# Performance work log

Measured on AMD Instinct MI355X. Metric: run time of the kernel, lower is better.

The kernel has to match this reference:

```python
import jax, jax.numpy as jnp
import numpy as np

TEMP = 0.07
MAX_SAMPLES = 2048
RADIUS = 10
HARD_FRAC = 0.75
FG_LABEL = 1
B, C, H, W = 8, 64, 256, 256
BLOCK = 32

MAX_FG = MAX_SAMPLES // 2                      # 1024
NEG_BUDGET = MAX_SAMPLES - MAX_FG              # 1024
HARD_BUDGET = int(round(HARD_FRAC * NEG_BUDGET))  # 768
RAND_BUDGET = NEG_BUDGET - HARD_BUDGET         # 256


def setup_inputs() -> dict:
    key = jax.random.key(0)
    feats = jax.random.normal(key, (B, C, H, W), dtype=jnp.float32)
    # 32x32-block checkerboard labels: guarantees abundant fg / ring / interior-bg pools
    ii, jj = jnp.meshgrid(jnp.arange(H), jnp.arange(W), indexing='ij')
    lbl = (((ii // BLOCK) + (jj // BLOCK)) % 2).astype(jnp.int32)
    labels = jnp.broadcast_to(lbl, (B, H, W))
    return {"feats": feats, "labels": labels}


def _forward(feats, labels):
    Bn, Cn, Hn, Wn = feats.shape
    n_pix = Hn * Wn
    f_flat = feats.reshape(Bn, Cn, n_pix).transpose(0, 2, 1)  # [B, P, C]
    l_flat = labels.reshape(Bn, n_pix)

    fg = labels == FG_LABEL                                   # [B, H, W]
    k = 2 * RADIUS + 1
    # max-pool dilation of fg mask (kernel k, stride 1, pad RADIUS == SAME)
    dil = jax.lax.reduce_window(fg.astype(jnp.float32), -jnp.inf, jax.lax.max,
                                (1, k, k), (1, 1, 1), 'SAME') > 0.0
    fg_flat = fg.reshape(Bn, n_pix)
    bg_flat = ~fg_flat                                        # all pixels valid (no ignore)
    ring_flat = dil.reshape(Bn, n_pix) & ~fg_flat & bg_flat
    bgonly_flat = bg_flat & ~ring_flat

    def per_image(f, y, fgm, ringm, bgm, key):
        k1, k2, k3 = jax.random.split(key, 3)
        def pick(mask, kk, n):
            # random subset of n true positions (== randperm[:n] in distribution)
            s = jnp.where(mask, jax.random.uniform(kk, mask.shape), -1.0)
            return jax.lax.top_k(s, n)[1]
        idx = jnp.concatenate([pick(fgm, k1, MAX_FG),
                               pick(ringm, k2, HARD_BUDGET),
                               pick(bgm, k3, RAND_BUDGET)])    # [K]
        fs = f[idx]                                            # [K, C]
        ys = y[idx]
        fs = fs / jnp.maximum(jnp.linalg.norm(fs, axis=1, keepdims=True), 1e-12)
        logits = fs @ fs.T / TEMP                              # [K, K]
        logits = logits - jax.lax.stop_gradient(logits.max(axis=1, keepdims=True))
        eye = jnp.eye(MAX_SAMPLES, dtype=bool)
        pos = (ys[:, None] == ys[None, :]) & ~eye
        exp_l = jnp.exp(logits) * (~eye)
        denom = jnp.maximum(exp_l.sum(axis=1), 1e-8)
        pos_sum = jnp.maximum(jnp.where(pos, exp_l, 0.0).sum(axis=1), 1e-8)
        valid = pos.any(axis=1) & (ys == FG_LABEL)
        loss_terms = -jnp.log(pos_sum / denom)
        n_valid = jnp.maximum(valid.sum(), 1)
        return jnp.where(valid, loss_terms, 0.0).sum() / n_valid

    keys = jax.random.split(jax.random.key(1), Bn)
    losses = jax.vmap(per_image)(f_flat, l_flat, fg_flat, ring_flat, bgonly_flat, keys)
    return losses.mean()


def reference(feats, labels):
    return _forward(feats, labels)
```

## Files before the change

### kernel.cpp

```cpp
#include <hip/hip_runtime.h>
#include <stdint.h>

#define NPIX   65536
#define NIMG   8
#define NCH    64
#define KSEL   2048
#define NFG    1024
#define NRING  768
#define NBG    256
#define INV_TEMP 14.285714285714286f

typedef __attribute__((ext_vector_type(8))) short bf16x8;
typedef __attribute__((ext_vector_type(4))) float f32x4;

__device__ __forceinline__ void tf2x32(uint32_t k0, uint32_t k1,
                                       uint32_t& x0, uint32_t& x1) {
  const uint32_t ks2 = k0 ^ k1 ^ 0x1BD11BDAu;
  x0 += k0; x1 += k1;
#define TF_RND(r) { x0 += x1; x1 = (x1 << (r)) | (x1 >> (32 - (r))); x1 ^= x0; }
  TF_RND(13) TF_RND(15) TF_RND(26) TF_RND(6)
  x0 += k1;  x1 += ks2 + 1u;
  TF_RND(17) TF_RND(29) TF_RND(16) TF_RND(24)
  x0 += ks2; x1 += k0 + 2u;
  TF_RND(13) TF_RND(15) TF_RND(26) TF_RND(6)
  x0 += k0;  x1 += k1 + 3u;
  TF_RND(17) TF_RND(29) TF_RND(16) TF_RND(24)
  x0 += k1;  x1 += ks2 + 4u;
  TF_RND(13) TF_RND(15) TF_RND(26) TF_RND(6)
  x0 += ks2; x1 += k0 + 5u;
#undef TF_RND
}

__device__ __forceinline__ ushort f2bf(float f) {
  uint32_t u = __float_as_uint(f);
  return (ushort)((u + 0x7FFFu + ((u >> 16) & 1u)) >> 16);
}

#define ZERO_F4 1552
__global__ __launch_bounds__(1024) void dilate_pack(const int* __restrict__ labels,
                                                    uint64_t* __restrict__ fgw,
                                                    uint64_t* __restrict__ dilw,
                                                    float4* __restrict__ zregion,
                                                    uint32_t* __restrict__ keys,
                                                    float* __restrict__ out) {
  __shared__ uint64_t fgs[336], hds[336];
  const int tid = threadIdx.x;
  const int img = blockIdx.x >> 2;
  const int r0 = (blockIdx.x & 3) * 64;

  if (blockIdx.x == 0) {
    for (int t = tid; t < ZERO_F4; t += 1024)
      zregion[t] = make_float4(0.f, 0.f, 0.f, 0.f);
  } else if (blockIdx.x == 1 && tid == 0) {
    out[0] = 0.0f;
    for (int b = 0; b < NIMG; ++b) {
      uint32_t kb0 = 0u, kb1 = (uint32_t)b;
      tf2x32(0u, 1u, kb0, kb1);
      for (int g = 0; g < 3; ++g) {
        uint32_t x0 = 0u, x1 = (uint32_t)g;
        tf2x32(kb0, kb1, x0, x1);
        keys[(b * 3 + g) * 2 + 0] = x0;
        keys[(b * 3 + g) * 2 + 1] = x1;
      }
    }
  }

  #pragma unroll
  for (int it = 0; it < 21; ++it) {
    int li = it * 1024 + tid;
    int hr = r0 - 10 + (li >> 8);
    int col = li & 255;
    bool bit = false;
    if (hr >= 0 && hr < 256) bit = (labels[(img << 16) + (hr << 8) + col] == 1);
    uint64_t m = __ballot(bit);
    if ((tid & 63) == 0) fgs[li >> 6] = m;
  }
  __syncthreads();

  for (int w = tid; w < 336; w += 1024) {
    int wc = w & 3;
    uint64_t x = fgs[w];
    uint64_t L = wc > 0 ? fgs[w - 1] : 0ull;
    uint64_t R = wc < 3 ? fgs[w + 1] : 0ull;
    uint64_t acc = x;
    #pragma unroll
    for (int s = 1; s <= 10; ++s) {
      acc |= (x << s) | (L >> (64 - s));
      acc |= (x >> s) | (R << (64 - s));
    }
    hds[w] = acc;
  }
  __syncthreads();

  for (int w = tid; w < 256; w += 1024) {
    int r = w >> 2, wc = w & 3;
    int gr = r0 + r;
    uint64_t acc = 0ull;
    #pragma unroll
    for (int dr = 0; dr <= 20; ++dr) acc |= hds[(r + dr) * 4 + wc];
    fgw[img * 1024 + gr * 4 + wc]  = fgs[(r + 10) * 4 + wc];
    dilw[img * 1024 + gr * 4 + wc] = acc;
  }
}

__global__ __launch_bounds__(256) void hash_hist(const uint64_t* __restrict__ fgw,
                                                 const uint64_t* __restrict__ dilw,
                                                 const uint32_t* __restrict__ keys,
                                                 uint32_t* __restrict__ mgrp,
                                                 uint32_t* __restrict__ hist) {
  __shared__ uint32_t lh[768];
  __shared__ uint64_t fgl[32], dll[32];
  const int tid = threadIdx.x;
  for (int t = tid; t < 768; t += 256) lh[t] = 0;
  const int b = blockIdx.x >> 5;
  const int base = blockIdx.x * 2048;
  const int w0 = (blockIdx.x & 31) * 32;
  if (tid < 32) fgl[tid] = fgw[b * 1024 + w0 + tid];
  else if (tid < 64) dll[tid - 32] = dilw[b * 1024 + w0 + tid - 32];
  const uint32_t K00 = keys[b * 6 + 0], K01 = keys[b * 6 + 1];
  const uint32_t K10 = keys[b * 6 + 2], K11 = keys[b * 6 + 3];
  const uint32_t K20 = keys[b * 6 + 4], K21 = keys[b * 6 + 5];
  __syncthreads();

  #pragma unroll
  for (int k = 0; k < 8; ++k) {
    int off = k * 256 + tid;
    int pix = (base + off) & 65535;
    int lw = off >> 6, bp = off & 63;
    uint32_t fgbit = (uint32_t)((fgl[lw] >> bp) & 1ull);
    uint32_t dilbit = (uint32_t)((dll[lw] >> bp) & 1ull);
    uint32_t grp = fgbit ? 0u : (dilbit ? 1u : 2u);
    uint32_t k0 = grp == 0 ? K00 : grp == 1 ? K10 : K20;
    uint32_t k1 = grp == 0 ? K01 : grp == 1 ? K11 : K21;
    uint32_t x0 = 0u, x1 = (uint32_t)pix;
    tf2x32(k0, k1, x0, x1);
    uint32_t m = (x0 ^ x1) >> 9;
    mgrp[base + off] = (m << 2) | grp;
    atomicAdd(&lh[grp * 256 + (m >> 15)], 1u);
  }
  __syncthreads();
  for (int t = tid; t < 768; t += 256)
    if (lh[t]) atomicAdd(&hist[b * 768 + t], lh[t]);
}

__global__ __launch_bounds__(256) void topk_emit(const uint32_t* __restrict__ mgrp,
                                                 const uint32_t* __restrict__ hist,
                                                 uint32_t* __restrict__ TG,
                                                 uint32_t* __restrict__ cnt,
                                                 uint32_t* __restrict__ candcnt,
                                                 unsigned long long* __restrict__ cand,
                                                 int* __restrict__ idx_out) {
  __shared__ uint32_t hh[768];
  __shared__ uint32_t sT[3], loc[3], lbd[3], basA[3], basB[3];
  const int tid = threadIdx.x;
  const int b = blockIdx.x >> 5;
  const int base = blockIdx.x * 2048;
  for (int t = tid; t < 768; t += 256) hh[t] = hist[b * 768 + t];
  if (tid < 3) { loc[tid] = 0; lbd[tid] = 0; }
  __syncthreads();

  if (tid < 3) {
    uint32_t nsel = tid == 0 ? NFG : tid == 1 ? NRING : NBG;
    const uint32_t* h = hh + tid * 256;
    uint32_t cum = 0; int T = 255;
    for (; T > 0; --T) {
      uint32_t c = h[T];
      if (cum + c >= nsel) break;
      cum += c;
    }
    sT[tid] = (uint32_t)T;
    if ((blockIdx.x & 31) == 0) {
      TG[(b * 3 + tid) * 2] = (uint32_t)T;
      TG[(b * 3 + tid) * 2 + 1] = cum;
    }
  }
  __syncthreads();
  const uint32_t T0 = sT[0], T1 = sT[1], T2 = sT[2];

  #pragma unroll
  for (int k = 0; k < 8; ++k) {
    uint32_t v = mgrp[base + k * 256 + tid];
    uint32_t g = v & 3u, bin = v >> 17;
    uint32_t T = g == 0 ? T0 : g == 1 ? T1 : T2;
    if (bin > T) atomicAdd(&loc[g], 1u);
    else if (bin == T) atomicAdd(&lbd[g], 1u);
  }
  __syncthreads();
  if (tid < 3) {
    basA[tid] = atomicAdd(&cnt[b * 3 + tid], loc[tid]);
    basB[tid] = atomicAdd(&candcnt[b * 3 + tid], lbd[tid]);
    loc[tid] = 0; lbd[tid] = 0;
  }
  __syncthreads();

  #pragma unroll
  for (int k = 0; k < 8; ++k) {
    int p = base + k * 256 + tid;
    uint32_t v = mgrp[p];
    uint32_t g = v & 3u, bin = v >> 17;
    uint32_t T = g == 0 ? T0 : g == 1 ? T1 : T2;
    int pix = p & 65535;
    if (bin > T) {
      uint32_t o = atomicAdd(&loc[g], 1u);
      int seg = g == 0 ? 0 : g == 1 ? NFG : (NFG + NRING);
      idx_out[b * KSEL + seg + (int)(basA[g] + o)] = pix;
    } else if (bin == T) {
      uint32_t o = atomicAdd(&lbd[g], 1u);
      uint32_t c = basB[g] + o;
      uint32_t m = v >> 2;
      if (c < 1024u)
        cand[(b * 3 + g) * 1024 + c] = ((unsigned long long)m << 16) | (uint32_t)pix;
    }
  }
}

#define GA 16
__global__ __launch_bounds__(256) void gather_rank_t(
    const float* __restrict__ feats, const int* __restrict__ idx,
    const uint32_t* __restrict__ TG, const uint32_t* __restrict__ candcnt,
    const unsigned long long* __restrict__ cand, ushort* __restrict__ fs) {
  __shared__ float tile[GA * 65];
  __shared__ float ssb[16 * GA];
  __shared__ float sscale[GA];
  __shared__ int lidx[GA];
  __shared__ unsigned long long cb[1024];
  const int tid = threadIdx.x;
  const int img = blockIdx.x >> 7;
  const int win = (blockIdx.x & 127) * GA;
  int seg, segoff, nsel;
  if (win < NFG)               { seg = 0; segoff = 0;            nsel = NFG; }
  else if (win < NFG + NRING)  { seg = 1; segoff = NFG;          nsel = NRING; }
  else                         { seg = 2; segoff = NFG + NRING;  nsel = NBG; }
  const int task = img * 3 + seg;
  const uint32_t G = TG[task * 2 + 1];
  const int poslo = win - segoff;

  if (tid < GA) {
    if ((uint32_t)(poslo + tid) < G)
      lidx[tid] = idx[img * KSEL + win + tid];
  }
  const bool needRank = (uint32_t)(poslo + GA) > G;
  if (needRank) {
    const int c = (int)(candcnt[task] < 1024u ? candcnt[task] : 1024u);
    const int r = nsel - (int)G;
    for (int i = tid; i < c; i += 256) cb[i] = cand[task * 1024 + i];
    __syncthreads();
    for (int i = tid; i < c; i += 256) {
      unsigned long long me = cb[i];
      uint32_t mm = (uint32_t)(me >> 16), pi = (uint32_t)(me & 0xFFFFu);
      int rank = 0;
      for (int j = 0; j < c; ++j) {
        unsigned long long o = cb[j];
        uint32_t om = (uint32_t)(o >> 16), op = (uint32_t)(o & 0xFFFFu);
        if (om > mm || (om == mm && op < pi)) ++rank;
      }
      if (rank < r) {
        int slot = (int)G + rank - poslo;
        if (slot >= 0 && slot < GA) lidx[slot] = (int)pi;
      }
    }
  }
  __syncthreads();

  const int a = tid & 15, q = tid >> 4;
  const int pix = lidx[a];
  const float* fb = feats + ((size_t)img * NCH + q * 4) * NPIX + pix;
  float ss = 0.f;
  #pragma unroll
  for (int k = 0; k < 4; ++k) {
    float v = fb[(size_t)k * NPIX];
    tile[a * 65 + q * 4 + k] = v;
    ss += v * v;
  }
  ssb[q * GA + a] = ss;
  __syncthreads();
  if (q == 0) {
    float tot = 0.f;
    #pragma unroll
    for (int q2 = 0; q2 < 16; ++q2) tot += ssb[q2 * GA + a];
    sscale[a] = 1.0f / fmaxf(sqrtf(tot), 1e-12f);
  }
  __syncthreads();

  const int row = tid >> 4, c4 = tid & 15;
  const float sc = sscale[row];
  ushort4 v4;
  v4.x = f2bf(tile[row * 65 + c4 * 4 + 0] * sc);
  v4.y = f2bf(tile[row * 65 + c4 * 4 + 1] * sc);
  v4.z = f2bf(tile[row * 65 + c4 * 4 + 2] * sc);
  v4.w = f2bf(tile[row * 65 + c4 * 4 + 3] * sc);
  ((ushort4*)(fs + ((size_t)img * KSEL + win + row) * NCH))[c4] = v4;
}

__global__ __launch_bounds__(256) void loss_mfma(const ushort* __restrict__ fs,
                                                 float* __restrict__ out) {
  const int img = blockIdx.x & 7;
  const int a0 = (blockIdx.x >> 3) * 32;
  const ushort* X = fs + (size_t)img * KSEL * NCH;
  const int tid = threadIdx.x;
  const int lane = tid & 63, wave = tid >> 6;
  const int quad = lane >> 4, col = lane & 15;
  const int rt = wave >> 1, colh = wave & 1;

  __shared__ float redD[2][2][16];
  __shared__ float redP[2][16];

  const int arow = a0 + rt * 16 + col;
  const bf16x8* Ap = (const bf16x8*)(X + (size_t)arow * NCH + quad * 8);
  const bf16x8 a_lo = Ap[0];
  const bf16x8 a_hi = Ap[4];

  float pD[4] = {0.f, 0.f, 0.f, 0.f};
  float pP[4] = {0.f, 0.f, 0.f, 0.f};
  const int ct0 = colh * 64;
  const int mbase = a0 + rt * 16 + quad * 4;

  for (int ct = ct0; ct < ct0 + 64; ++ct) {
    const int j = ct * 16 + col;
    const bf16x8* Bp = (const bf16x8*)(X + (size_t)j * NCH + quad * 8);
    bf16x8 b_lo = Bp[0];
    bf16x8 b_hi = Bp[4];
    f32x4 d = {0.f, 0.f, 0.f, 0.f};
    d = __builtin_amdgcn_mfma_f32_16x16x32_bf16(a_lo, b_lo, d, 0, 0, 0);
    d = __builtin_amdgcn_mfma_f32_16x16x32_bf16(a_hi, b_hi, d, 0, 0, 0);
    #pragma unroll
    for (int r = 0; r < 4; ++r) {
      float e = __expf(d[r] * INV_TEMP);
      if (j == mbase + r) e = 0.f;
      pD[r] += e;
      if (colh == 0) pP[r] += e;
    }
  }

  #pragma unroll
  for (int o = 1; o < 16; o <<= 1) {
    #pragma unroll
    for (int r = 0; r < 4; ++r) {
      pD[r] += __shfl_xor(pD[r], o);
      pP[r] += __shfl_xor(pP[r], o);
    }
  }
  if (col == 0) {
    #pragma unroll
    for (int r = 0; r < 4; ++r) {
      redD[rt][colh][quad * 4 + r] = pD[r];
      if (colh == 0) redP[rt][quad * 4 + r] = pP[r];
    }
  }
  __syncthreads();

  float term = 0.f;
  if (tid < 32) {
    int lrt = tid >> 4, lr = tid & 15;
    float dsum = fmaxf(redD[lrt][0][lr] + redD[lrt][1][lr], 1e-8f);
    float psum = fmaxf(redP[lrt][lr], 1e-8f);
    term = __logf(dsum) - __logf(psum);
  }
  if (tid < 64) {
    #pragma unroll
    for (int o = 32; o > 0; o >>= 1) term += __shfl_xor(term, o);
    if (tid == 0) atomicAdd(out, term * (1.0f / (NFG * NIMG)));
  }
}

extern "C" void kernel_launch(void* const* d_in, const int* in_sizes, int n_in,
                              void* d_out, int out_size, void* d_ws, size_t ws_size,
                              hipStream_t stream) {
  const float* feats = (const float*)d_in[0];
  const int* labels  = (const int*)d_in[1];
  float* out = (float*)d_out;

  char* ws = (char*)d_ws;
  uint64_t* fgw     = (uint64_t*)(ws);
  uint64_t* dilw    = (uint64_t*)(ws + 65536);
  uint32_t* keys    = (uint32_t*)(ws + 131072);
  uint32_t* TG      = (uint32_t*)(ws + 131328);
  uint32_t* hist    = (uint32_t*)(ws + 131584);
  uint32_t* cnt     = (uint32_t*)(ws + 156160);
  uint32_t* candcnt = (uint32_t*)(ws + 156288);
  unsigned long long* cand = (unsigned long long*)(ws + 156416);
  int*      idx     = (int*)(ws + 353024);
  uint32_t* mgrp    = (uint32_t*)(ws + 524288);
  ushort*   fs      = (ushort*)(ws + 2621440);

  hipLaunchKernelGGL(dilate_pack, dim3(32), dim3(1024), 0, stream,
                     labels, fgw, dilw, (float4*)hist, keys, out);
  hipLaunchKernelGGL(hash_hist, dim3(NIMG * 32), dim3(256), 0, stream,
                     fgw, dilw, keys, mgrp, hist);
  hipLaunchKernelGGL(topk_emit, dim3(NIMG * 32), dim3(256), 0, stream,
                     mgrp, hist, TG, cnt, candcnt, cand, idx);
  hipLaunchKernelGGL(gather_rank_t, dim3((NIMG * KSEL) / GA), dim3(256), 0, stream,
                     feats, idx, TG, candcnt, cand, fs);
  hipLaunchKernelGGL(loss_mfma, dim3(NIMG * (NFG / 32)), dim3(256), 0, stream,
                     fs, out);
}
```

Before: 243.0 us.

## Fuse dilation into hashing and replace random gather with streaming compaction

Merges the dilation and hash/histogram kernels into one per-band kernel with per-block histograms in place of global atomics. Instead of scattered per-pixel feature gathers, topk now writes a pixel-to-slot map. A new kernel streams every feature plane coalesced and scatters the selected values into a compact buffer, and a normalise kernel reads that buffer and writes bf16 rows. This trades random 4-byte reads across 64 strided channels for reading the whole 134MB feature tensor sequentially, plus a larger zeroing pass for the map.

```diff
diff --git a/kernel.cpp b/kernel.cpp
--- a/kernel.cpp
+++ b/kernel.cpp
@@ -9,6 +9,10 @@
 #define NRING  768
 #define NBG    256
 #define INV_TEMP 14.285714285714286f
+
+#define FTC    5120
+#define ZERO_F4 65552
+#define ZERO_PER_BLK 257
 
 typedef __attribute__((ext_vector_type(8))) short bf16x8;
 typedef __attribute__((ext_vector_type(4))) float f32x4;
@@ -36,48 +40,47 @@
   return (ushort)((u + 0x7FFFu + ((u >> 16) & 1u)) >> 16);
 }
 
-#define ZERO_F4 1552
-__global__ __launch_bounds__(1024) void dilate_pack(const int* __restrict__ labels,
-                                                    uint64_t* __restrict__ fgw,
-                                                    uint64_t* __restrict__ dilw,
-                                                    float4* __restrict__ zregion,
-                                                    uint32_t* __restrict__ keys,
-                                                    float* __restrict__ out) {
-  __shared__ uint64_t fgs[336], hds[336];
+__global__ __launch_bounds__(256) void prep_hash(const int* __restrict__ labels,
+                                                 float4* __restrict__ zreg,
+                                                 uint32_t* __restrict__ mgrp,
+                                                 uint32_t* __restrict__ hist32,
+                                                 float* __restrict__ out) {
+  __shared__ uint64_t fgs[112], hds[112], fgb[32], dlb[32];
+  __shared__ uint32_t lh[768];
+  __shared__ uint32_t skeys[6];
   const int tid = threadIdx.x;
-  const int img = blockIdx.x >> 2;
-  const int r0 = (blockIdx.x & 3) * 64;
-
-  if (blockIdx.x == 0) {
-    for (int t = tid; t < ZERO_F4; t += 1024)
-      zregion[t] = make_float4(0.f, 0.f, 0.f, 0.f);
-  } else if (blockIdx.x == 1 && tid == 0) {
-    out[0] = 0.0f;
-    for (int b = 0; b < NIMG; ++b) {
-      uint32_t kb0 = 0u, kb1 = (uint32_t)b;
-      tf2x32(0u, 1u, kb0, kb1);
-      for (int g = 0; g < 3; ++g) {
-        uint32_t x0 = 0u, x1 = (uint32_t)g;
-        tf2x32(kb0, kb1, x0, x1);
-        keys[(b * 3 + g) * 2 + 0] = x0;
-        keys[(b * 3 + g) * 2 + 1] = x1;
-      }
-    }
-  }
-
-  #pragma unroll
-  for (int it = 0; it < 21; ++it) {
-    int li = it * 1024 + tid;
-    int hr = r0 - 10 + (li >> 8);
-    int col = li & 255;
+  const int img = blockIdx.x >> 5;
+  const int band = blockIdx.x & 31;
+
+  {
+    int start = blockIdx.x * ZERO_PER_BLK;
+    int end = start + ZERO_PER_BLK; if (end > ZERO_F4) end = ZERO_F4;
+    for (int i = start + tid; i < end; i += 256)
+      zreg[i] = make_float4(0.f, 0.f, 0.f, 0.f);
+  }
+  if (blockIdx.x == 0 && tid == 0) out[0] = 0.0f;
+
+  if (tid < 3) {
+    uint32_t kb0 = 0u, kb1 = (uint32_t)img;
+    tf2x32(0u, 1u, kb0, kb1);
+    uint32_t x0 = 0u, x1 = (uint32_t)tid;
+    tf2x32(kb0, kb1, x0, x1);
+    skeys[tid * 2 + 0] = x0;
+    skeys[tid * 2 + 1] = x1;
+  }
+  for (int t = tid; t < 768; t += 256) lh[t] = 0;
+
+  const int rbase = band * 8 - 10;
+  for (int it = 0; it < 28; ++it) {
+    int hr = rbase + it;
     bool bit = false;
-    if (hr >= 0 && hr < 256) bit = (labels[(img << 16) + (hr << 8) + col] == 1);
+    if (hr >= 0 && hr < 256) bit = (labels[(img << 16) + (hr << 8) + tid] == 1);
     uint64_t m = __ballot(bit);
-    if ((tid & 63) == 0) fgs[li >> 6] = m;
-  }
-  __syncthreads();
-
-  for (int w = tid; w < 336; w += 1024) {
+    if ((tid & 63) == 0) fgs[it * 4 + (tid >> 6)] = m;
+  }
+  __syncthreads();
+
+  for (int w = tid; w < 112; w += 256) {
     int wc = w & 3;
     uint64_t x = fgs[w];
     uint64_t L = wc > 0 ? fgs[w - 1] : 0ull;
@@ -92,70 +95,60 @@
   }
   __syncthreads();
 
-  for (int w = tid; w < 256; w += 1024) {
+  for (int w = tid; w < 32; w += 256) {
     int r = w >> 2, wc = w & 3;
-    int gr = r0 + r;
     uint64_t acc = 0ull;
     #pragma unroll
     for (int dr = 0; dr <= 20; ++dr) acc |= hds[(r + dr) * 4 + wc];
-    fgw[img * 1024 + gr * 4 + wc]  = fgs[(r + 10) * 4 + wc];
-    dilw[img * 1024 + gr * 4 + wc] = acc;
-  }
-}
-
-__global__ __launch_bounds__(256) void hash_hist(const uint64_t* __restrict__ fgw,
-                                                 const uint64_t* __restrict__ dilw,
-                                                 const uint32_t* __restrict__ keys,
-                                                 uint32_t* __restrict__ mgrp,
-                                                 uint32_t* __restrict__ hist) {
-  __shared__ uint32_t lh[768];
-  __shared__ uint64_t fgl[32], dll[32];
-  const int tid = threadIdx.x;
-  for (int t = tid; t < 768; t += 256) lh[t] = 0;
-  const int b = blockIdx.x >> 5;
-  const int base = blockIdx.x * 2048;
-  const int w0 = (blockIdx.x & 31) * 32;
-  if (tid < 32) fgl[tid] = fgw[b * 1024 + w0 + tid];
-  else if (tid < 64) dll[tid - 32] = dilw[b * 1024 + w0 + tid - 32];
-  const uint32_t K00 = keys[b * 6 + 0], K01 = keys[b * 6 + 1];
-  const uint32_t K10 = keys[b * 6 + 2], K11 = keys[b * 6 + 3];
-  const uint32_t K20 = keys[b * 6 + 4], K21 = keys[b * 6 + 5];
-  __syncthreads();
+    fgb[w] = fgs[(r + 10) * 4 + wc];
+    dlb[w] = acc;
+  }
+  __syncthreads();
+
+  const uint32_t K00 = skeys[0], K01 = skeys[1];
+  const uint32_t K10 = skeys[2], K11 = skeys[3];
+  const uint32_t K20 = skeys[4], K21 = skeys[5];
+  const int pbase = blockIdx.x * 2048;
 
   #pragma unroll
   for (int k = 0; k < 8; ++k) {
     int off = k * 256 + tid;
-    int pix = (base + off) & 65535;
+    int pix = (pbase + off) & 65535;
     int lw = off >> 6, bp = off & 63;
-    uint32_t fgbit = (uint32_t)((fgl[lw] >> bp) & 1ull);
-    uint32_t dilbit = (uint32_t)((dll[lw] >> bp) & 1ull);
+    uint32_t fgbit = (uint32_t)((fgb[lw] >> bp) & 1ull);
+    uint32_t dilbit = (uint32_t)((dlb[lw] >> bp) & 1ull);
     uint32_t grp = fgbit ? 0u : (dilbit ? 1u : 2u);
     uint32_t k0 = grp == 0 ? K00 : grp == 1 ? K10 : K20;
     uint32_t k1 = grp == 0 ? K01 : grp == 1 ? K11 : K21;
     uint32_t x0 = 0u, x1 = (uint32_t)pix;
     tf2x32(k0, k1, x0, x1);
     uint32_t m = (x0 ^ x1) >> 9;
-    mgrp[base + off] = (m << 2) | grp;
+    mgrp[pbase + off] = (m << 2) | grp;
     atomicAdd(&lh[grp * 256 + (m >> 15)], 1u);
   }
   __syncthreads();
-  for (int t = tid; t < 768; t += 256)
-    if (lh[t]) atomicAdd(&hist[b * 768 + t], lh[t]);
-}
-
-__global__ __launch_bounds__(256) void topk_emit(const uint32_t* __restrict__ mgrp,
-                                                 const uint32_t* __restrict__ hist,
-                                                 uint32_t* __restrict__ TG,
-                                                 uint32_t* __restrict__ cnt,
-                                                 uint32_t* __restrict__ candcnt,
-                                                 unsigned long long* __restrict__ cand,
-                                                 int* __restrict__ idx_out) {
+  for (int t = tid; t < 768; t += 256) hist32[blockIdx.x * 768 + t] = lh[t];
+}
+
+__global__ __launch_bounds__(256) void topk_map(const uint32_t* __restrict__ mgrp,
+                                                const uint32_t* __restrict__ hist32,
+                                                uint32_t* __restrict__ TG,
+                                                uint32_t* __restrict__ cnt,
+                                                uint32_t* __restrict__ candcnt,
+                                                unsigned long long* __restrict__ cand,
+                                                ushort* __restrict__ map) {
   __shared__ uint32_t hh[768];
   __shared__ uint32_t sT[3], loc[3], lbd[3], basA[3], basB[3];
   const int tid = threadIdx.x;
   const int b = blockIdx.x >> 5;
   const int base = blockIdx.x * 2048;
-  for (int t = tid; t < 768; t += 256) hh[t] = hist[b * 768 + t];
+  for (int t = tid; t < 768; t += 256) {
+    uint32_t s = 0;
+    const uint32_t* hp = hist32 + (size_t)b * 32 * 768 + t;
+    #pragma unroll
+    for (int band = 0; band < 32; ++band) s += hp[band * 768];
+    hh[t] = s;
+  }
   if (tid < 3) { loc[tid] = 0; lbd[tid] = 0; }
   __syncthreads();
 
@@ -202,50 +195,65 @@
     int pix = p & 65535;
     if (bin > T) {
       uint32_t o = atomicAdd(&loc[g], 1u);
-      int seg = g == 0 ? 0 : g == 1 ? NFG : (NFG + NRING);
-      idx_out[b * KSEL + seg + (int)(basA[g] + o)] = pix;
+      int segb = g == 0 ? 0 : g == 1 ? NFG : (NFG + NRING);
+      map[(b << 16) + pix] = (ushort)(segb + (int)(basA[g] + o) + 1);
     } else if (bin == T) {
       uint32_t o = atomicAdd(&lbd[g], 1u);
       uint32_t c = basB[g] + o;
       uint32_t m = v >> 2;
-      if (c < 1024u)
-        cand[(b * 3 + g) * 1024 + c] = ((unsigned long long)m << 16) | (uint32_t)pix;
-    }
-  }
-}
-
-#define GA 16
-__global__ __launch_bounds__(256) void gather_rank_t(
-    const float* __restrict__ feats, const int* __restrict__ idx,
-    const uint32_t* __restrict__ TG, const uint32_t* __restrict__ candcnt,
-    const unsigned long long* __restrict__ cand, ushort* __restrict__ fs) {
-  __shared__ float tile[GA * 65];
-  __shared__ float ssb[16 * GA];
-  __shared__ float sscale[GA];
-  __shared__ int lidx[GA];
+      if (c < 1024u) {
+        cand[((size_t)b * 3 + g) * 1024 + c] =
+            ((unsigned long long)m << 16) | (uint32_t)pix;
+        map[(b << 16) + pix] = (ushort)(2048 + (int)g * 1024 + (int)c + 1);
+      }
+    }
+  }
+}
+
+__global__ __launch_bounds__(256) void stream_compact(const float* __restrict__ feats,
+                                                      const ushort* __restrict__ map,
+                                                      float* __restrict__ ft) {
+  const int img = blockIdx.x & 7;
+  const int ch = blockIdx.x >> 3;
+  const float4* plane = (const float4*)(feats + ((size_t)(img * 64 + ch)) * NPIX);
+  const uint2* m4 = (const uint2*)(map + (size_t)img * NPIX);
+  float* fto = ft + (size_t)(img * 64 + ch) * FTC;
+  for (int i = threadIdx.x; i < NPIX / 4; i += 256) {
+    float4 v = plane[i];
+    uint2 mm = m4[i];
+    uint32_t s;
+    s = mm.x & 0xFFFFu; if (s) fto[s - 1] = v.x;
+    s = mm.x >> 16;     if (s) fto[s - 1] = v.y;
+    s = mm.y & 0xFFFFu; if (s) fto[s - 1] = v.z;
+    s = mm.y >> 16;     if (s) fto[s - 1] = v.w;
+  }
+}
+
+__global__ __launch_bounds__(128) void norm_write(const float* __restrict__ ft,
+                                                  const uint32_t* __restrict__ TG,
+                                                  const uint32_t* __restrict__ candcnt,
+                                                  const unsigned long long* __restrict__ cand,
+                                                  ushort* __restrict__ fs) {
   __shared__ unsigned long long cb[1024];
+  __shared__ ushort rk2j[1024];
   const int tid = threadIdx.x;
-  const int img = blockIdx.x >> 7;
-  const int win = (blockIdx.x & 127) * GA;
-  int seg, segoff, nsel;
-  if (win < NFG)               { seg = 0; segoff = 0;            nsel = NFG; }
-  else if (win < NFG + NRING)  { seg = 1; segoff = NFG;          nsel = NRING; }
-  else                         { seg = 2; segoff = NFG + NRING;  nsel = NBG; }
-  const int task = img * 3 + seg;
+  const int img = blockIdx.x & 7;
+  const int tile = blockIdx.x >> 3;
+  const int s0 = tile * 128;
+  int g, segb, nsel;
+  if (tile < 8)       { g = 0; segb = 0;           nsel = NFG; }
+  else if (tile < 14) { g = 1; segb = NFG;         nsel = NRING; }
+  else                { g = 2; segb = NFG + NRING; nsel = NBG; }
+  const int task = img * 3 + g;
   const uint32_t G = TG[task * 2 + 1];
-  const int poslo = win - segoff;
-
-  if (tid < GA) {
-    if ((uint32_t)(poslo + tid) < G)
-      lidx[tid] = idx[img * KSEL + win + tid];
-  }
-  const bool needRank = (uint32_t)(poslo + GA) > G;
-  if (needRank) {
+  const int lo = s0 - segb;
+
+  if (lo + 127 >= (int)G) {
     const int c = (int)(candcnt[task] < 1024u ? candcnt[task] : 1024u);
     const int r = nsel - (int)G;
-    for (int i = tid; i < c; i += 256) cb[i] = cand[task * 1024 + i];
+    for (int i = tid; i < c; i += 128) cb[i] = cand[(size_t)task * 1024 + i];
     __syncthreads();
-    for (int i = tid; i < c; i += 256) {
+    for (int i = tid; i < c; i += 128) {
       unsigned long long me = cb[i];
       uint32_t mm = (uint32_t)(me >> 16), pi = (uint32_t)(me & 0xFFFFu);
       int rank = 0;
@@ -254,42 +262,41 @@
         uint32_t om = (uint32_t)(o >> 16), op = (uint32_t)(o & 0xFFFFu);
         if (om > mm || (om == mm && op < pi)) ++rank;
       }
-      if (rank < r) {
-        int slot = (int)G + rank - poslo;
-        if (slot >= 0 && slot < GA) lidx[slot] = (int)pi;
-      }
-    }
-  }
-  __syncthreads();
-
-  const int a = tid & 15, q = tid >> 4;
-  const int pix = lidx[a];
-  const float* fb = feats + ((size_t)img * NCH + q * 4) * NPIX + pix;
-  float ss = 0.f;
-  #pragma unroll
-  for (int k = 0; k < 4; ++k) {
-    float v = fb[(size_t)k * NPIX];
-    tile[a * 65 + q * 4 + k] = v;
-    ss += v * v;
-  }
-  ssb[q * GA + a] = ss;
-  __syncthreads();
-  if (q == 0) {
-    float tot = 0.f;
-    #pragma unroll
-    for (int q2 = 0; q2 < 16; ++q2) tot += ssb[q2 * GA + a];
-    sscale[a] = 1.0f / fmaxf(sqrtf(tot), 1e-12f);
-  }
-  __syncthreads();
-
-  const int row = tid >> 4, c4 = tid & 15;
-  const float sc = sscale[row];
-  ushort4 v4;
-  v4.x = f2bf(tile[row * 65 + c4 * 4 + 0] * sc);
-  v4.y = f2bf(tile[row * 65 + c4 * 4 + 1] * sc);
-  v4.z = f2bf(tile[row * 65 + c4 * 4 + 2] * sc);
-  v4.w = f2bf(tile[row * 65 + c4 * 4 + 3] * sc);
-  ((ushort4*)(fs + ((size_t)img * KSEL + win + row) * NCH))[c4] = v4;
+      if (rank < r) rk2j[rank] = (ushort)i;
+    }
+    __syncthreads();
+  }
+
+  const int sl = lo + tid;
+  int col;
+  if (sl < (int)G) col = s0 + tid;
+  else col = 2048 + g * 1024 + (int)rk2j[sl - (int)G];
+
+  const float* fb = ft + (size_t)img * 64 * FTC + col;
+  float v[64];
+  float tot = 0.f;
+  #pragma unroll
+  for (int q = 0; q < 16; ++q) {
+    float ss = 0.f;
+    #pragma unroll
+    for (int k = 0; k < 4; ++k) {
+      float x = fb[(size_t)(q * 4 + k) * FTC];
+      v[q * 4 + k] = x;
+      ss += x * x;
+    }
+    tot += ss;
+  }
+  const float sc = 1.0f / fmaxf(sqrtf(tot), 1e-12f);
+  ushort* row = fs + ((size_t)img * KSEL + s0 + tid) * NCH;
+  #pragma unroll
+  for (int c4 = 0; c4 < 16; ++c4) {
+    ushort4 o4;
+    o4.x = f2bf(v[c4 * 4 + 0] * sc);
+    o4.y = f2bf(v[c4 * 4 + 1] * sc);
+    o4.z = f2bf(v[c4 * 4 + 2] * sc);
+    o4.w = f2bf(v[c4 * 4 + 3] * sc);
+    ((ushort4*)row)[c4] = o4;
+  }
 }
 
 __global__ __launch_bounds__(256) void loss_mfma(const ushort* __restrict__ fs,
@@ -371,26 +378,25 @@
   float* out = (float*)d_out;
 
   char* ws = (char*)d_ws;
-  uint64_t* fgw     = (uint64_t*)(ws);
-  uint64_t* dilw    = (uint64_t*)(ws + 65536);
-  uint32_t* keys    = (uint32_t*)(ws + 131072);
-  uint32_t* TG      = (uint32_t*)(ws + 131328);
-  uint32_t* hist    = (uint32_t*)(ws + 131584);
-  uint32_t* cnt     = (uint32_t*)(ws + 156160);
-  uint32_t* candcnt = (uint32_t*)(ws + 156288);
-  unsigned long long* cand = (unsigned long long*)(ws + 156416);
-  int*      idx     = (int*)(ws + 353024);
-  uint32_t* mgrp    = (uint32_t*)(ws + 524288);
-  ushort*   fs      = (ushort*)(ws + 2621440);
-
-  hipLaunchKernelGGL(dilate_pack, dim3(32), dim3(1024), 0, stream,
-                     labels, fgw, dilw, (float4*)hist, keys, out);
-  hipLaunchKernelGGL(hash_hist, dim3(NIMG * 32), dim3(256), 0, stream,
-                     fgw, dilw, keys, mgrp, hist);
-  hipLaunchKernelGGL(topk_emit, dim3(NIMG * 32), dim3(256), 0, stream,
-                     mgrp, hist, TG, cnt, candcnt, cand, idx);
-  hipLaunchKernelGGL(gather_rank_t, dim3((NIMG * KSEL) / GA), dim3(256), 0, stream,
-                     feats, idx, TG, candcnt, cand, fs);
+  uint32_t* TG      = (uint32_t*)(ws);
+  uint32_t* cnt     = (uint32_t*)(ws + 4096);
+  uint32_t* candcnt = (uint32_t*)(ws + 4224);
+  ushort*   map     = (ushort*)(ws + 4352);
+  float4*   zreg    = (float4*)(ws + 4096);
+  unsigned long long* cand = (unsigned long long*)(ws + 1052928);
+  uint32_t* mgrp    = (uint32_t*)(ws + 2097152);
+  uint32_t* hist32  = (uint32_t*)(ws + 4194304);
+  float*    ft      = (float*)(ws + 8388608);
+  ushort*   fs      = (ushort*)(ws + 18874368);
+
+  hipLaunchKernelGGL(prep_hash, dim3(NIMG * 32), dim3(256), 0, stream,
+                     labels, zreg, mgrp, hist32, out);
+  hipLaunchKernelGGL(topk_map, dim3(NIMG * 32), dim3(256), 0, stream,
+                     mgrp, hist32, TG, cnt, candcnt, cand, map);
+  hipLaunchKernelGGL(stream_compact, dim3(NCH * NIMG), dim3(256), 0, stream,
+                     feats, map, ft);
+  hipLaunchKernelGGL(norm_write, dim3(NIMG * 16), dim3(128), 0, stream,
+                     ft, TG, candcnt, cand, fs);
   hipLaunchKernelGGL(loss_mfma, dim3(NIMG * (NFG / 32)), dim3(256), 0, stream,
                      fs, out);
 }
```

Measured after the change: 332.4 us. +36.8%, slower.

## Fuse dilation and hash-histogram kernels with per-block partial histograms

Applied to the files above, without the earlier changes.

Merges the dilate_pack and hash_hist kernels into one prep_hash kernel. Each 256-thread block recomputes its 8-row band dilation, including the 10-row halo, locally in shared memory, and derives the per-image RNG keys itself. The global histogram atomics are replaced by per-block partial histograms, which topk_emit then sums over 32 bands. This removes one launch and the fgw/dilw global round trip. The cost is redundant halo label loads and an extra reduction read in topk_emit.

```diff
diff --git a/kernel.cpp b/kernel.cpp
--- a/kernel.cpp
+++ b/kernel.cpp
@@ -36,48 +36,44 @@
   return (ushort)((u + 0x7FFFu + ((u >> 16) & 1u)) >> 16);
 }
 
-#define ZERO_F4 1552
-__global__ __launch_bounds__(1024) void dilate_pack(const int* __restrict__ labels,
-                                                    uint64_t* __restrict__ fgw,
-                                                    uint64_t* __restrict__ dilw,
-                                                    float4* __restrict__ zregion,
-                                                    uint32_t* __restrict__ keys,
-                                                    float* __restrict__ out) {
-  __shared__ uint64_t fgs[336], hds[336];
+__global__ __launch_bounds__(256) void prep_hash(const int* __restrict__ labels,
+                                                 float4* __restrict__ zreg,
+                                                 uint32_t* __restrict__ mgrp,
+                                                 uint32_t* __restrict__ hist32,
+                                                 float* __restrict__ out) {
+  __shared__ uint64_t fgs[112], hds[112], fgb[32], dlb[32];
+  __shared__ uint32_t lh[768];
+  __shared__ uint32_t skeys[6];
   const int tid = threadIdx.x;
-  const int img = blockIdx.x >> 2;
-  const int r0 = (blockIdx.x & 3) * 64;
+  const int img = blockIdx.x >> 5;
+  const int band = blockIdx.x & 31;
 
   if (blockIdx.x == 0) {
-    for (int t = tid; t < ZERO_F4; t += 1024)
-      zregion[t] = make_float4(0.f, 0.f, 0.f, 0.f);
-  } else if (blockIdx.x == 1 && tid == 0) {
-    out[0] = 0.0f;
-    for (int b = 0; b < NIMG; ++b) {
-      uint32_t kb0 = 0u, kb1 = (uint32_t)b;
-      tf2x32(0u, 1u, kb0, kb1);
-      for (int g = 0; g < 3; ++g) {
-        uint32_t x0 = 0u, x1 = (uint32_t)g;
-        tf2x32(kb0, kb1, x0, x1);
-        keys[(b * 3 + g) * 2 + 0] = x0;
-        keys[(b * 3 + g) * 2 + 1] = x1;
-      }
-    }
-  }
-
-  #pragma unroll
-  for (int it = 0; it < 21; ++it) {
-    int li = it * 1024 + tid;
-    int hr = r0 - 10 + (li >> 8);
-    int col = li & 255;
+    if (tid < 16) zreg[tid] = make_float4(0.f, 0.f, 0.f, 0.f);
+    if (tid == 0) out[0] = 0.0f;
+  }
+
+  if (tid < 3) {
+    uint32_t kb0 = 0u, kb1 = (uint32_t)img;
+    tf2x32(0u, 1u, kb0, kb1);
+    uint32_t x0 = 0u, x1 = (uint32_t)tid;
+    tf2x32(kb0, kb1, x0, x1);
+    skeys[tid * 2 + 0] = x0;
+    skeys[tid * 2 + 1] = x1;
+  }
+  for (int t = tid; t < 768; t += 256) lh[t] = 0;
+
+  const int rbase = band * 8 - 10;
+  for (int it = 0; it < 28; ++it) {
+    int hr = rbase + it;
     bool bit = false;
-    if (hr >= 0 && hr < 256) bit = (labels[(img << 16) + (hr << 8) + col] == 1);
+    if (hr >= 0 && hr < 256) bit = (labels[(img << 16) + (hr << 8) + tid] == 1);
     uint64_t m = __ballot(bit);
-    if ((tid & 63) == 0) fgs[li >> 6] = m;
-  }
-  __syncthreads();
-
-  for (int w = tid; w < 336; w += 1024) {
+    if ((tid & 63) == 0) fgs[it * 4 + (tid >> 6)] = m;
+  }
+  __syncthreads();
+
+  for (int w = tid; w < 112; w += 256) {
     int wc = w & 3;
     uint64_t x = fgs[w];
     uint64_t L = wc > 0 ? fgs[w - 1] : 0ull;
@@ -92,59 +88,43 @@
   }
   __syncthreads();
 
-  for (int w = tid; w < 256; w += 1024) {
+  for (int w = tid; w < 32; w += 256) {
     int r = w >> 2, wc = w & 3;
-    int gr = r0 + r;
     uint64_t acc = 0ull;
     #pragma unroll
     for (int dr = 0; dr <= 20; ++dr) acc |= hds[(r + dr) * 4 + wc];
-    fgw[img * 1024 + gr * 4 + wc]  = fgs[(r + 10) * 4 + wc];
-    dilw[img * 1024 + gr * 4 + wc] = acc;
-  }
-}
-
-__global__ __launch_bounds__(256) void hash_hist(const uint64_t* __restrict__ fgw,
-                                                 const uint64_t* __restrict__ dilw,
-                                                 const uint32_t* __restrict__ keys,
-                                                 uint32_t* __restrict__ mgrp,
-                                                 uint32_t* __restrict__ hist) {
-  __shared__ uint32_t lh[768];
-  __shared__ uint64_t fgl[32], dll[32];
-  const int tid = threadIdx.x;
-  for (int t = tid; t < 768; t += 256) lh[t] = 0;
-  const int b = blockIdx.x >> 5;
-  const int base = blockIdx.x * 2048;
-  const int w0 = (blockIdx.x & 31) * 32;
-  if (tid < 32) fgl[tid] = fgw[b * 1024 + w0 + tid];
-  else if (tid < 64) dll[tid - 32] = dilw[b * 1024 + w0 + tid - 32];
-  const uint32_t K00 = keys[b * 6 + 0], K01 = keys[b * 6 + 1];
-  const uint32_t K10 = keys[b * 6 + 2], K11 = keys[b * 6 + 3];
-  const uint32_t K20 = keys[b * 6 + 4], K21 = keys[b * 6 + 5];
-  __syncthreads();
+    fgb[w] = fgs[(r + 10) * 4 + wc];
+    dlb[w] = acc;
+  }
+  __syncthreads();
+
+  const uint32_t K00 = skeys[0], K01 = skeys[1];
+  const uint32_t K10 = skeys[2], K11 = skeys[3];
+  const uint32_t K20 = skeys[4], K21 = skeys[5];
+  const int pbase = blockIdx.x * 2048;
 
   #pragma unroll
   for (int k = 0; k < 8; ++k) {
     int off = k * 256 + tid;
-    int pix = (base + off) & 65535;
+    int pix = (pbase + off) & 65535;
     int lw = off >> 6, bp = off & 63;
-    uint32_t fgbit = (uint32_t)((fgl[lw] >> bp) & 1ull);
-    uint32_t dilbit = (uint32_t)((dll[lw] >> bp) & 1ull);
+    uint32_t fgbit = (uint32_t)((fgb[lw] >> bp) & 1ull);
+    uint32_t dilbit = (uint32_t)((dlb[lw] >> bp) & 1ull);
     uint32_t grp = fgbit ? 0u : (dilbit ? 1u : 2u);
     uint32_t k0 = grp == 0 ? K00 : grp == 1 ? K10 : K20;
     uint32_t k1 = grp == 0 ? K01 : grp == 1 ? K11 : K21;
     uint32_t x0 = 0u, x1 = (uint32_t)pix;
     tf2x32(k0, k1, x0, x1);
     uint32_t m = (x0 ^ x1) >> 9;
-    mgrp[base + off] = (m << 2) | grp;
+    mgrp[pbase + off] = (m << 2) | grp;
     atomicAdd(&lh[grp * 256 + (m >> 15)], 1u);
   }
   __syncthreads();
-  for (int t = tid; t < 768; t += 256)
-    if (lh[t]) atomicAdd(&hist[b * 768 + t], lh[t]);
+  for (int t = tid; t < 768; t += 256) hist32[blockIdx.x * 768 + t] = lh[t];
 }
 
 __global__ __launch_bounds__(256) void topk_emit(const uint32_t* __restrict__ mgrp,
-                                                 const uint32_t* __restrict__ hist,
+                                                 const uint32_t* __restrict__ hist32,
                                                  uint32_t* __restrict__ TG,
                                                  uint32_t* __restrict__ cnt,
                                                  uint32_t* __restrict__ candcnt,
@@ -155,7 +135,13 @@
   const int tid = threadIdx.x;
   const int b = blockIdx.x >> 5;
   const int base = blockIdx.x * 2048;
-  for (int t = tid; t < 768; t += 256) hh[t] = hist[b * 768 + t];
+  for (int t = tid; t < 768; t += 256) {
+    uint32_t s = 0;
+    const uint32_t* hp = hist32 + (size_t)b * 32 * 768 + t;
+    #pragma unroll
+    for (int band = 0; band < 32; ++band) s += hp[band * 768];
+    hh[t] = s;
+  }
   if (tid < 3) { loc[tid] = 0; lbd[tid] = 0; }
   __syncthreads();
 
@@ -209,7 +195,8 @@
       uint32_t c = basB[g] + o;
       uint32_t m = v >> 2;
       if (c < 1024u)
-        cand[(b * 3 + g) * 1024 + c] = ((unsigned long long)m << 16) | (uint32_t)pix;
+        cand[((size_t)b * 3 + g) * 1024 + c] =
+            ((unsigned long long)m << 16) | (uint32_t)pix;
     }
   }
 }
@@ -371,24 +358,20 @@
   float* out = (float*)d_out;
 
   char* ws = (char*)d_ws;
-  uint64_t* fgw     = (uint64_t*)(ws);
-  uint64_t* dilw    = (uint64_t*)(ws + 65536);
-  uint32_t* keys    = (uint32_t*)(ws + 131072);
-  uint32_t* TG      = (uint32_t*)(ws + 131328);
-  uint32_t* hist    = (uint32_t*)(ws + 131584);
-  uint32_t* cnt     = (uint32_t*)(ws + 156160);
-  uint32_t* candcnt = (uint32_t*)(ws + 156288);
-  unsigned long long* cand = (unsigned long long*)(ws + 156416);
-  int*      idx     = (int*)(ws + 353024);
-  uint32_t* mgrp    = (uint32_t*)(ws + 524288);
-  ushort*   fs      = (ushort*)(ws + 2621440);
-
-  hipLaunchKernelGGL(dilate_pack, dim3(32), dim3(1024), 0, stream,
-                     labels, fgw, dilw, (float4*)hist, keys, out);
-  hipLaunchKernelGGL(hash_hist, dim3(NIMG * 32), dim3(256), 0, stream,
-                     fgw, dilw, keys, mgrp, hist);
+  uint32_t* TG      = (uint32_t*)(ws);
+  uint32_t* cnt     = (uint32_t*)(ws + 4096);
+  uint32_t* candcnt = (uint32_t*)(ws + 4224);
+  float4*   zreg    = (float4*)(ws + 4096);
+  unsigned long long* cand = (unsigned long long*)(ws + 8192);
+  int*      idx     = (int*)(ws + 262144);
+  uint32_t* mgrp    = (uint32_t*)(ws + 2097152);
+  uint32_t* hist32  = (uint32_t*)(ws + 4194304);
+  ushort*   fs      = (ushort*)(ws + 8388608);
+
+  hipLaunchKernelGGL(prep_hash, dim3(NIMG * 32), dim3(256), 0, stream,
+                     labels, zreg, mgrp, hist32, out);
   hipLaunchKernelGGL(topk_emit, dim3(NIMG * 32), dim3(256), 0, stream,
-                     mgrp, hist, TG, cnt, candcnt, cand, idx);
+                     mgrp, hist32, TG, cnt, candcnt, cand, idx);
   hipLaunchKernelGGL(gather_rank_t, dim3((NIMG * KSEL) / GA), dim3(256), 0, stream,
                      feats, idx, TG, candcnt, cand, fs);
   hipLaunchKernelGGL(loss_mfma, dim3(NIMG * (NFG / 32)), dim3(256), 0, stream,
```

New measurement: 239.9 us. Within noise of the previous version (-1.3%).
